# Optimization experiments

Hardware: AMD Instinct MI355X
Metric: run time of the kernel (lower is better)

## Reference

```python
import jax, jax.numpy as jnp
import numpy as np

N = 100000   # nodes
E = 1600000  # edges (no self loops; added per PyG default)
DIN = 64; DMID = 64; DOUT = 64; H = 8
C_MID = DMID // H  # per-head dim for concat layers
NEG_SLOPE = 0.2


def _segment_softmax(logits, seg, num):
    # logits: [E', H], seg: [E'] target node ids
    m = jax.ops.segment_max(logits, seg, num_segments=num)  # [N, H]
    e = jnp.exp(logits - m[seg])
    s = jax.ops.segment_sum(e, seg, num_segments=num)
    return e / (s[seg] + 1e-16)


def _gatv2_layer(x, src, dst, Wl, Wr, att, bias, heads, concat):
    n = x.shape[0]
    c = Wl.shape[1] // heads
    xl = (x @ Wl).reshape(n, heads, c)  # source transform
    xr = (x @ Wr).reshape(n, heads, c)  # target transform
    m = xl[src] + xr[dst]               # [E', H, C] gathered messages
    e = jnp.where(m > 0, m, NEG_SLOPE * m)
    alpha = jnp.einsum('ehc,hc->eh', e, att)            # [E', H]
    alpha = _segment_softmax(alpha, dst, n)
    out = jax.ops.segment_sum(alpha[..., None] * xl[src], dst, num_segments=n)  # [N, H, C]
    if concat:
        out = out.reshape(n, heads * c)
    else:
        out = out.mean(axis=1)
    return out + bias


def setup_inputs() -> dict:
    key = jax.random.key(0)
    ks = jax.random.split(key, 16)
    x = jax.random.normal(ks[0], (N, DIN), jnp.float32)
    src = jax.random.randint(ks[1], (E,), 0, N)
    dst = jax.random.randint(ks[2], (E,), 0, N)
    dst = jnp.where(src == dst, (dst + 1) % N, dst)  # no pre-existing self loops
    edge_index = jnp.stack([src, dst]).astype(jnp.int64)

    def lin(k, fi, fo):
        return jax.random.normal(k, (fi, fo), jnp.float32) / np.sqrt(fi)

    inp = {'x': x, 'edge_index': edge_index}
    # layer 0: din -> H*C_MID (concat), layer 1: dmid -> H*C_MID (concat), layer 2: dmid -> H*DOUT (mean)
    dims = [(DIN, H * C_MID, C_MID), (DMID, H * C_MID, C_MID), (DMID, H * DOUT, DOUT)]
    kidx = 3
    for i, (fi, fo, c) in enumerate(dims):
        inp[f'W{i}l'] = lin(ks[kidx], fi, fo); kidx += 1
        inp[f'W{i}r'] = lin(ks[kidx], fi, fo); kidx += 1
        inp[f'a{i}'] = jax.random.normal(ks[kidx], (H, c), jnp.float32) / np.sqrt(c); kidx += 1
        bsize = fo if i < 2 else DOUT
        inp[f'b{i}'] = jnp.zeros((bsize,), jnp.float32)
    return inp


def reference(x, edge_index, W0l, W0r, a0, b0, W1l, W1r, a1, b1, W2l, W2r, a2, b2):
    # add self loops (PyG GATv2Conv default add_self_loops=True)
    loop = jnp.arange(N, dtype=edge_index.dtype)
    src = jnp.concatenate([edge_index[0], loop])
    dst = jnp.concatenate([edge_index[1], loop])

    # eval mode: dropout is identity
    h = jax.nn.elu(_gatv2_layer(x, src, dst, W0l, W0r, a0, b0, H, True))
    prev_h = jnp.zeros_like(h)

    h_in = h + prev_h
    h = jax.nn.elu(_gatv2_layer(h_in, src, dst, W1l, W1r, a1, b1, H, True))
    prev_h = h_in

    h_in = h + prev_h
    out = _gatv2_layer(h_in, src, dst, W2l, W2r, a2, b2, H, False)
    return out
```

## Files before the change

### kernel.cpp

```cpp
#include <hip/hip_runtime.h>
#include <math.h>

#define NNODES 100000
typedef unsigned short bf16_t;

typedef __attribute__((ext_vector_type(8))) short bf16x8;
typedef __attribute__((ext_vector_type(4))) float f32x4;

#define LOG2E 1.44269504f
#define THR2 11.5415603f

__device__ __forceinline__ float bf_lo(unsigned u) { return __uint_as_float(u << 16); }
__device__ __forceinline__ float bf_hi(unsigned u) { return __uint_as_float(u & 0xffff0000u); }
__device__ __forceinline__ bf16_t f2bf(float f) {
  unsigned u = __float_as_uint(f);
  return (bf16_t)((u + 0x7fffu + ((u >> 16) & 1u)) >> 16);
}
__device__ __forceinline__ float leaky(float v) { return fmaxf(v, 0.2f * v); }

#define LDK 68

__global__ __launch_bounds__(256) void gemm_mfma(const float* __restrict__ in,
                                                 const float* __restrict__ Wl,
                                                 const float* __restrict__ Wr,
                                                 bf16_t* __restrict__ XL,
                                                 bf16_t* __restrict__ XR,
                                                 int n, int fo, int col0, int ncols) {
  __shared__ bf16_t sX[64][LDK];
  __shared__ bf16_t sL[64][LDK];
  __shared__ bf16_t sR[64][LDK];
  int r0 = blockIdx.x * 64;
  int ct = blockIdx.y * 64;
  for (int i = threadIdx.x; i < 64 * 64; i += 256) {
    int r = i >> 6, k = i & 63;
    float v = (r0 + r < n) ? in[(size_t)(r0 + r) * 64 + k] : 0.f;
    sX[r][k] = f2bf(v);
  }
  for (int i = threadIdx.x; i < 64 * 64; i += 256) {
    int k = i >> 6, c = i & 63;
    int gc = col0 + ct + c;
    sL[c][k] = f2bf(Wl[k * fo + gc]);
    sR[c][k] = f2bf(Wr[k * fo + gc]);
  }
  __syncthreads();
  int w = threadIdx.x >> 6, l = threadIdx.x & 63;
  int l16 = l & 15, kg = l >> 4;
  bf16x8 a0 = *(const bf16x8*)&sX[w * 16 + l16][kg * 8];
  bf16x8 a1 = *(const bf16x8*)&sX[w * 16 + l16][kg * 8 + 32];
  f32x4 accL[4], accR[4];
#pragma unroll
  for (int nt = 0; nt < 4; ++nt) {
#pragma unroll
    for (int r = 0; r < 4; ++r) { accL[nt][r] = 0.f; accR[nt][r] = 0.f; }
  }
#pragma unroll
  for (int nt = 0; nt < 4; ++nt) {
    bf16x8 bl0 = *(const bf16x8*)&sL[nt * 16 + l16][kg * 8];
    bf16x8 bl1 = *(const bf16x8*)&sL[nt * 16 + l16][kg * 8 + 32];
    bf16x8 br0 = *(const bf16x8*)&sR[nt * 16 + l16][kg * 8];
    bf16x8 br1 = *(const bf16x8*)&sR[nt * 16 + l16][kg * 8 + 32];
    accL[nt] = __builtin_amdgcn_mfma_f32_16x16x32_bf16(a0, bl0, accL[nt], 0, 0, 0);
    accL[nt] = __builtin_amdgcn_mfma_f32_16x16x32_bf16(a1, bl1, accL[nt], 0, 0, 0);
    accR[nt] = __builtin_amdgcn_mfma_f32_16x16x32_bf16(a0, br0, accR[nt], 0, 0, 0);
    accR[nt] = __builtin_amdgcn_mfma_f32_16x16x32_bf16(a1, br1, accR[nt], 0, 0, 0);
  }
#pragma unroll
  for (int nt = 0; nt < 4; ++nt) {
#pragma unroll
    for (int r = 0; r < 4; ++r) {
      int grow = r0 + w * 16 + kg * 4 + r;
      if (grow < n) {
        size_t o = (size_t)grow * ncols + ct + nt * 16 + l16;
        XL[o] = f2bf(accL[nt][r]);
        XR[o] = f2bf(accR[nt][r]);
      }
    }
  }
}

__global__ void zeroi(int* __restrict__ p, int n) {
  int i = blockIdx.x * blockDim.x + threadIdx.x;
  if (i < n) p[i] = 0;
}
__global__ void histrank(const int* __restrict__ ei, int E,
                         int* __restrict__ cnt, unsigned char* __restrict__ rank) {
  int e = blockIdx.x * blockDim.x + threadIdx.x;
  if (e < E) rank[e] = (unsigned char)atomicAdd(&cnt[ei[E + e]], 1);
}
__global__ void scan1(const int* __restrict__ cnt, int n,
                      int* __restrict__ scn, int* __restrict__ bsum) {
  __shared__ int sh[256];
  int t = threadIdx.x, i = blockIdx.x * 256 + t;
  int v = (i < n) ? cnt[i] : 0;
  sh[t] = v;
  __syncthreads();
  for (int off = 1; off < 256; off <<= 1) {
    int x = (t >= off) ? sh[t - off] : 0;
    __syncthreads();
    sh[t] += x;
    __syncthreads();
  }
  if (i < n) scn[i] = sh[t];
  if (t == 255) bsum[blockIdx.x] = sh[255];
}
__global__ void scan2(int* __restrict__ bsum, int nb) {
  __shared__ int sh[512];
  int t = threadIdx.x;
  sh[t] = (t < nb) ? bsum[t] : 0;
  __syncthreads();
  for (int off = 1; off < 512; off <<= 1) {
    int x = (t >= off) ? sh[t - off] : 0;
    __syncthreads();
    sh[t] += x;
    __syncthreads();
  }
  if (t < nb) bsum[t] = sh[t];
}
__global__ void scan3(int* __restrict__ RS, const int* __restrict__ bsum, int n) {
  int i = blockIdx.x * blockDim.x + threadIdx.x;
  if (i >= n) return;
  int b = i >> 8;
  int pre = (b > 0) ? bsum[b - 1] : 0;
  RS[i + 1] += pre;
  if (i == 0) RS[0] = 0;
}
__global__ void scat2(const int* __restrict__ ei, int E,
                      const int* __restrict__ RS,
                      const unsigned char* __restrict__ rank,
                      int* __restrict__ SRC) {
  int e = blockIdx.x * blockDim.x + threadIdx.x;
  if (e >= E) return;
  int d = ei[E + e];
  SRC[RS[d] + (int)rank[e]] = ei[e];
}

__global__ __launch_bounds__(256) void fused01(const bf16_t* __restrict__ xl,
                                               const bf16_t* __restrict__ xr,
                                               const float* __restrict__ att,
                                               const int* __restrict__ RS,
                                               const int* __restrict__ SRC,
                                               const float* __restrict__ bias,
                                               float* __restrict__ curbuf,
                                               int n, int addres) {
  int l = threadIdx.x & 63;
  int q = l & 15;
  int d = blockIdx.x * 16 + ((threadIdx.x >> 6) << 2) + (l >> 4);
  int dd = (d < n) ? d : 0;
  float a0 = att[4 * q] * LOG2E, a1 = att[4 * q + 1] * LOG2E;
  float a2 = att[4 * q + 2] * LOG2E, a3 = att[4 * q + 3] * LOG2E;
  const char* xlb = (const char*)xl;
  uint2 ur = *(const uint2*)((const char*)xr + ((unsigned)dd << 7) + (q << 3));
  float r0 = bf_lo(ur.x), r1 = bf_hi(ur.x), r2 = bf_lo(ur.y), r3 = bf_hi(ur.y);
  int rs = RS[dd], re = RS[dd + 1];
  int cnt = (d < n) ? (re - rs + 1) : 0;
  int mc = max(cnt, __shfl_xor(cnt, 16));
  mc = max(mc, __shfl_xor(mc, 32));
  float m = -1e30f, s = 0.f, ac0 = 0.f, ac1 = 0.f, ac2 = 0.f, ac3 = 0.f;
  int nsid = (rs < re) ? SRC[rs] : dd;
  uint2 u = *(const uint2*)(xlb + ((unsigned)dd << 7) + (q << 3));
  for (int j = 0;;) {
    uint2 un = *(const uint2*)(xlb + ((unsigned)nsid << 7) + (q << 3));
    int i2 = rs + j + 1;
    int nn = (i2 < re) ? SRC[i2] : dd;
    float x0 = bf_lo(u.x), x1 = bf_hi(u.x), x2 = bf_lo(u.y), x3 = bf_hi(u.y);
    float t = leaky(x0 + r0) * a0 + leaky(x1 + r1) * a1 +
              leaky(x2 + r2) * a2 + leaky(x3 + r3) * a3;
    t += __shfl_xor(t, 1);
    if (j >= cnt) t = -1e30f;
    if (__any(t > m + THR2)) {
      float nm = fmaxf(m, t);
      float e0 = exp2f(m - nm);
      s *= e0; ac0 *= e0; ac1 *= e0; ac2 *= e0; ac3 *= e0; m = nm;
    }
    float e1 = exp2f(t - m);
    s += e1;
    ac0 += e1 * x0; ac1 += e1 * x1; ac2 += e1 * x2; ac3 += e1 * x3;
    ++j;
    if (j >= mc) break;
    u = un;
    nsid = nn;
  }
  if (d < n) {
    float inv = 1.f / (s + 1e-16f);
    float v0 = ac0 * inv + bias[4 * q];
    float v1 = ac1 * inv + bias[4 * q + 1];
    float v2 = ac2 * inv + bias[4 * q + 2];
    float v3 = ac3 * inv + bias[4 * q + 3];
    v0 = v0 > 0.f ? v0 : expm1f(v0);
    v1 = v1 > 0.f ? v1 : expm1f(v1);
    v2 = v2 > 0.f ? v2 : expm1f(v2);
    v3 = v3 > 0.f ? v3 : expm1f(v3);
    float4* pc = (float4*)(curbuf + (size_t)d * 64 + 4 * q);
    if (addres) {
      float4 pr = *pc;
      v0 += pr.x; v1 += pr.y; v2 += pr.z; v3 += pr.w;
    }
    *pc = make_float4(v0, v1, v2, v3);
  }
}

template <int NH>
__global__ __launch_bounds__(256) void fused2(const bf16_t* __restrict__ xl,
                                              const bf16_t* __restrict__ xr,
                                              const float* __restrict__ att,
                                              const int* __restrict__ RS,
                                              const int* __restrict__ SRC,
                                              const float* __restrict__ bias,
                                              float* __restrict__ accbuf,
                                              float* __restrict__ outbuf,
                                              int n, int h0, int pass) {
  const int LPD = NH * 8;
  const unsigned RB = NH * 128u;
  int l = threadIdx.x & 63;
  int ll = l & (LPD - 1);
  int d = blockIdx.x * (256 / LPD) + (threadIdx.x >> 6) * (64 / LPD) +
          (NH == 4 ? (l >> 5) : 0);
  int dd = (d < n) ? d : 0;
  int h = ll >> 3, c0 = (ll & 7) * 8;
  const float* ap = att + (h0 + h) * 64 + c0;
  float a[8];
#pragma unroll
  for (int k = 0; k < 8; ++k) a[k] = ap[k] * LOG2E;
  const char* xlb = (const char*)xl;
  uint4 ur = *(const uint4*)((const char*)xr + (unsigned)dd * RB + (ll << 4));
  float r[8] = {bf_lo(ur.x), bf_hi(ur.x), bf_lo(ur.y), bf_hi(ur.y),
                bf_lo(ur.z), bf_hi(ur.z), bf_lo(ur.w), bf_hi(ur.w)};
  int rs = RS[dd], re = RS[dd + 1];
  int cnt = (d < n) ? (re - rs + 1) : 0;
  int maxcnt = (NH == 4) ? max(cnt, __shfl_xor(cnt, 32)) : cnt;
  float m = -1e30f, s = 0.f;
  float ac[8] = {0.f, 0.f, 0.f, 0.f, 0.f, 0.f, 0.f, 0.f};
  int nsid = (rs < re) ? SRC[rs] : dd;
  uint4 u = *(const uint4*)(xlb + (unsigned)dd * RB + (ll << 4));
  for (int j = 0;;) {
    uint4 un = *(const uint4*)(xlb + (unsigned)nsid * RB + (ll << 4));
    int i2 = rs + j + 1;
    int nn = (i2 < re) ? SRC[i2] : dd;
    float x[8] = {bf_lo(u.x), bf_hi(u.x), bf_lo(u.y), bf_hi(u.y),
                  bf_lo(u.z), bf_hi(u.z), bf_lo(u.w), bf_hi(u.w)};
    float t = 0.f;
#pragma unroll
    for (int k = 0; k < 8; ++k) t += leaky(x[k] + r[k]) * a[k];
    t += __shfl_xor(t, 1);
    t += __shfl_xor(t, 2);
    t += __shfl_xor(t, 4);
    if (j >= cnt) t = -1e30f;
    if (__any(t > m + THR2)) {
      float nm = fmaxf(m, t);
      float e0 = exp2f(m - nm);
      s *= e0;
#pragma unroll
      for (int k = 0; k < 8; ++k) ac[k] *= e0;
      m = nm;
    }
    float e1 = exp2f(t - m);
    s += e1;
#pragma unroll
    for (int k = 0; k < 8; ++k) ac[k] += e1 * x[k];
    ++j;
    if (j >= maxcnt) break;
    u = un;
    nsid = nn;
  }
  float inv = 1.f / (s + 1e-16f);
  float v[8];
#pragma unroll
  for (int k = 0; k < 8; ++k) {
    v[k] = ac[k] * inv;
    v[k] += __shfl_xor(v[k], 8);
    v[k] += __shfl_xor(v[k], 16);
    if (NH == 8) v[k] += __shfl_xor(v[k], 32);
  }
  if (ll < 8 && d < n) {
    if (NH == 8) {
      const float* bp = bias + ll * 8;
      float4 o0, o1;
      o0.x = v[0] * 0.125f + bp[0];
      o0.y = v[1] * 0.125f + bp[1];
      o0.z = v[2] * 0.125f + bp[2];
      o0.w = v[3] * 0.125f + bp[3];
      o1.x = v[4] * 0.125f + bp[4];
      o1.y = v[5] * 0.125f + bp[5];
      o1.z = v[6] * 0.125f + bp[6];
      o1.w = v[7] * 0.125f + bp[7];
      float* po = outbuf + (size_t)d * 64 + ll * 8;
      *(float4*)po = o0;
      *(float4*)(po + 4) = o1;
    } else {
      float* pa = accbuf + (size_t)d * 64 + ll * 8;
      if (pass == 0) {
        *(float4*)pa = make_float4(v[0], v[1], v[2], v[3]);
        *(float4*)(pa + 4) = make_float4(v[4], v[5], v[6], v[7]);
      } else {
        float4 p0 = *(float4*)pa;
        float4 p1 = *(float4*)(pa + 4);
        const float* bp = bias + ll * 8;
        float4 o0, o1;
        o0.x = (p0.x + v[0]) * 0.125f + bp[0];
        o0.y = (p0.y + v[1]) * 0.125f + bp[1];
        o0.z = (p0.z + v[2]) * 0.125f + bp[2];
        o0.w = (p0.w + v[3]) * 0.125f + bp[3];
        o1.x = (p1.x + v[4]) * 0.125f + bp[4];
        o1.y = (p1.y + v[5]) * 0.125f + bp[5];
        o1.z = (p1.z + v[6]) * 0.125f + bp[6];
        o1.w = (p1.w + v[7]) * 0.125f + bp[7];
        float* po = outbuf + (size_t)d * 64 + ll * 8;
        *(float4*)po = o0;
        *(float4*)(po + 4) = o1;
      }
    }
  }
}

extern "C" void kernel_launch(void* const* d_in, const int* in_sizes, int n_in,
                              void* d_out, int out_size, void* d_ws, size_t ws_size,
                              hipStream_t stream) {
  const float* x = (const float*)d_in[0];
  const int* ei = (const int*)d_in[1];
  const float* Wmat[3][2] = {
      {(const float*)d_in[2], (const float*)d_in[3]},
      {(const float*)d_in[6], (const float*)d_in[7]},
      {(const float*)d_in[10], (const float*)d_in[11]}};
  const float* att[3] = {(const float*)d_in[4], (const float*)d_in[8],
                         (const float*)d_in[12]};
  const float* bias[3] = {(const float*)d_in[5], (const float*)d_in[9],
                          (const float*)d_in[13]};
  const int N = NNODES;
  int E = in_sizes[1] / 2;

  auto al = [](size_t b) { return (b + 255) & ~(size_t)255; };
  size_t csr_bytes = al((size_t)(N + 1) * 4) + al((size_t)N * 4) + al(512 * 4) +
                     al((size_t)E * 4) + al((size_t)E);
  size_t need8 = al((size_t)N * 64 * 4) + 2 * al((size_t)N * 512 * 2) + csr_bytes;
  bool mode8 = (ws_size >= need8);

  char* p = (char*)d_ws;
  auto alloc = [&](size_t bytes) {
    char* r = p;
    p += (bytes + 255) & ~(size_t)255;
    return r;
  };
  float* CUR = (float*)alloc((size_t)N * 64 * 4);
  size_t xtab = mode8 ? (size_t)N * 512 * 2 : (size_t)N * 256 * 2;
  bf16_t* XL = (bf16_t*)alloc(xtab);
  bf16_t* XR = (bf16_t*)alloc(xtab);
  int* RS = (int*)alloc((size_t)(N + 1) * 4);
  int* CNT = (int*)alloc((size_t)N * 4);
  int* BSUM = (int*)alloc(512 * 4);
  int* SRC = (int*)alloc((size_t)E * 4);
  unsigned char* RANK = (unsigned char*)alloc((size_t)E);
  float* ACC = mode8 ? nullptr : (float*)alloc((size_t)N * 64 * 4);

  const int nb = (N + 255) / 256;
  const int geblk = (E + 255) / 256;
  const int g01 = (N + 15) / 16;
  const int gx64 = (N + 63) / 64;

  zeroi<<<nb, 256, 0, stream>>>(CNT, N);
  histrank<<<geblk, 256, 0, stream>>>(ei, E, CNT, RANK);
  scan1<<<nb, 256, 0, stream>>>(CNT, N, RS + 1, BSUM);
  scan2<<<1, 512, 0, stream>>>(BSUM, nb);
  scan3<<<nb, 256, 0, stream>>>(RS, BSUM, N);
  scat2<<<geblk, 256, 0, stream>>>(ei, E, RS, RANK, SRC);

  for (int layer = 0; layer < 2; ++layer) {
    const float* in = (layer == 0) ? x : CUR;
    gemm_mfma<<<dim3(gx64, 1), 256, 0, stream>>>(in, Wmat[layer][0], Wmat[layer][1],
                                                 XL, XR, N, 64, 0, 64);
    fused01<<<g01, 256, 0, stream>>>(XL, XR, att[layer], RS, SRC, bias[layer],
                                     CUR, N, layer);
  }

  if (mode8) {
    gemm_mfma<<<dim3(gx64, 8), 256, 0, stream>>>(CUR, Wmat[2][0], Wmat[2][1],
                                                 XL, XR, N, 512, 0, 512);
    fused2<8><<<(N + 3) / 4, 256, 0, stream>>>(XL, XR, att[2], RS, SRC, bias[2],
                                               nullptr, (float*)d_out, N, 0, 0);
  } else {
    for (int hb = 0; hb < 2; ++hb) {
      gemm_mfma<<<dim3(gx64, 4), 256, 0, stream>>>(CUR, Wmat[2][0], Wmat[2][1],
                                                   XL, XR, N, 512, hb * 256, 256);
      fused2<4><<<(N + 7) / 8, 256, 0, stream>>>(XL, XR, att[2], RS, SRC, bias[2],
                                                 ACC, (float*)d_out, N, hb * 4, hb);
    }
  }
}
```

Measured before the change: 632.2 us.

## Split leaky-ReLU attention into linear per-node terms plus abs edge term

Uses leaky(v) = 0.6v + 0.4|v| to move the linear part of the attention score into per-node scalars AL/AR, computed in the GEMM epilogue and stored in new small tables. The edge loop then only evaluates the abs term and adds two gathered scalars. It also swaps exp2f for raw v_exp_f32, adds an occupancy hint to the launch bounds, and drops the j>=cnt mask in the 8-head path. The cost is an extra gathered AL load per edge, and the abs/linear split and bf16-rounded inputs to the per-node terms can shift results slightly.

```diff
diff --git a/kernel.cpp b/kernel.cpp
--- a/kernel.cpp
+++ b/kernel.cpp
@@ -9,6 +9,8 @@
 
 #define LOG2E 1.44269504f
 #define THR2 11.5415603f
+#define CLIN (0.6f * LOG2E)
+#define CABS (0.4f * LOG2E)
 
 __device__ __forceinline__ float bf_lo(unsigned u) { return __uint_as_float(u << 16); }
 __device__ __forceinline__ float bf_hi(unsigned u) { return __uint_as_float(u & 0xffff0000u); }
@@ -16,15 +18,23 @@
   unsigned u = __float_as_uint(f);
   return (bf16_t)((u + 0x7fffu + ((u >> 16) & 1u)) >> 16);
 }
-__device__ __forceinline__ float leaky(float v) { return fmaxf(v, 0.2f * v); }
+__device__ __forceinline__ float ex2(float x) {
+  float r;
+  asm("v_exp_f32 %0, %1" : "=v"(r) : "v"(x));
+  return r;
+}
 
 #define LDK 68
 
+template <int HM>
 __global__ __launch_bounds__(256) void gemm_mfma(const float* __restrict__ in,
                                                  const float* __restrict__ Wl,
                                                  const float* __restrict__ Wr,
+                                                 const float* __restrict__ att,
                                                  bf16_t* __restrict__ XL,
                                                  bf16_t* __restrict__ XR,
+                                                 float* __restrict__ AL,
+                                                 float* __restrict__ AR,
                                                  int n, int fo, int col0, int ncols) {
   __shared__ bf16_t sX[64][LDK];
   __shared__ bf16_t sL[64][LDK];
@@ -64,15 +74,49 @@
     accR[nt] = __builtin_amdgcn_mfma_f32_16x16x32_bf16(a0, br0, accR[nt], 0, 0, 0);
     accR[nt] = __builtin_amdgcn_mfma_f32_16x16x32_bf16(a1, br1, accR[nt], 0, 0, 0);
   }
-#pragma unroll
-  for (int nt = 0; nt < 4; ++nt) {
-#pragma unroll
-    for (int r = 0; r < 4; ++r) {
-      int grow = r0 + w * 16 + kg * 4 + r;
-      if (grow < n) {
+  float aw[4];
+#pragma unroll
+  for (int nt = 0; nt < 4; ++nt) aw[nt] = att[col0 + ct + nt * 16 + l16] * CLIN;
+  int head1 = (col0 + ct) >> 6;
+#pragma unroll
+  for (int r = 0; r < 4; ++r) {
+    int grow = r0 + w * 16 + kg * 4 + r;
+    bool ok = grow < n;
+    float sLh = 0.f, sRh = 0.f;
+#pragma unroll
+    for (int nt = 0; nt < 4; ++nt) {
+      bf16_t bl = f2bf(accL[nt][r]), br = f2bf(accR[nt][r]);
+      float xl_ = bf_lo((unsigned)bl << 16 >> 16 << 16);
+      float xr_ = bf_lo((unsigned)br);
+      xl_ = __uint_as_float(((unsigned)bl) << 16);
+      xr_ = __uint_as_float(((unsigned)br) << 16);
+      if (ok) {
         size_t o = (size_t)grow * ncols + ct + nt * 16 + l16;
-        XL[o] = f2bf(accL[nt][r]);
-        XR[o] = f2bf(accR[nt][r]);
+        XL[o] = bl;
+        XR[o] = br;
+      }
+      if (HM) {
+        sLh += aw[nt] * xl_;
+        sRh += aw[nt] * xr_;
+      } else {
+        float vL = aw[nt] * xl_, vR = aw[nt] * xr_;
+        vL += __shfl_xor(vL, 1); vL += __shfl_xor(vL, 2); vL += __shfl_xor(vL, 4);
+        vR += __shfl_xor(vR, 1); vR += __shfl_xor(vR, 2); vR += __shfl_xor(vR, 4);
+        if ((l16 & 7) == 0 && ok) {
+          int head = 2 * nt + (l16 >> 3);
+          AL[grow * 8 + head] = vL;
+          AR[grow * 8 + head] = vR;
+        }
+      }
+    }
+    if (HM) {
+      sLh += __shfl_xor(sLh, 1); sLh += __shfl_xor(sLh, 2);
+      sLh += __shfl_xor(sLh, 4); sLh += __shfl_xor(sLh, 8);
+      sRh += __shfl_xor(sRh, 1); sRh += __shfl_xor(sRh, 2);
+      sRh += __shfl_xor(sRh, 4); sRh += __shfl_xor(sRh, 8);
+      if (l16 == 0 && ok) {
+        AL[grow * 8 + head1] = sLh;
+        AR[grow * 8 + head1] = sRh;
       }
     }
   }
@@ -134,23 +178,27 @@
   SRC[RS[d] + (int)rank[e]] = ei[e];
 }
 
-__global__ __launch_bounds__(256) void fused01(const bf16_t* __restrict__ xl,
-                                               const bf16_t* __restrict__ xr,
-                                               const float* __restrict__ att,
-                                               const int* __restrict__ RS,
-                                               const int* __restrict__ SRC,
-                                               const float* __restrict__ bias,
-                                               float* __restrict__ curbuf,
-                                               int n, int addres) {
+__global__ __launch_bounds__(256, 6) void fused01(const bf16_t* __restrict__ xl,
+                                                  const bf16_t* __restrict__ xr,
+                                                  const float* __restrict__ att,
+                                                  const float* __restrict__ AL,
+                                                  const float* __restrict__ AR,
+                                                  const int* __restrict__ RS,
+                                                  const int* __restrict__ SRC,
+                                                  const float* __restrict__ bias,
+                                                  float* __restrict__ curbuf,
+                                                  int n, int addres) {
   int l = threadIdx.x & 63;
   int q = l & 15;
+  int h01 = q >> 1;
   int d = blockIdx.x * 16 + ((threadIdx.x >> 6) << 2) + (l >> 4);
   int dd = (d < n) ? d : 0;
-  float a0 = att[4 * q] * LOG2E, a1 = att[4 * q + 1] * LOG2E;
-  float a2 = att[4 * q + 2] * LOG2E, a3 = att[4 * q + 3] * LOG2E;
+  float c0 = att[4 * q] * CABS, c1 = att[4 * q + 1] * CABS;
+  float c2 = att[4 * q + 2] * CABS, c3 = att[4 * q + 3] * CABS;
   const char* xlb = (const char*)xl;
   uint2 ur = *(const uint2*)((const char*)xr + ((unsigned)dd << 7) + (q << 3));
   float r0 = bf_lo(ur.x), r1 = bf_hi(ur.x), r2 = bf_lo(ur.y), r3 = bf_hi(ur.y);
+  float ard = AR[dd * 8 + h01];
   int rs = RS[dd], re = RS[dd + 1];
   int cnt = (d < n) ? (re - rs + 1) : 0;
   int mc = max(cnt, __shfl_xor(cnt, 16));
@@ -158,26 +206,30 @@
   float m = -1e30f, s = 0.f, ac0 = 0.f, ac1 = 0.f, ac2 = 0.f, ac3 = 0.f;
   int nsid = (rs < re) ? SRC[rs] : dd;
   uint2 u = *(const uint2*)(xlb + ((unsigned)dd << 7) + (q << 3));
+  float alc = AL[dd * 8 + h01];
   for (int j = 0;;) {
     uint2 un = *(const uint2*)(xlb + ((unsigned)nsid << 7) + (q << 3));
+    float aln = AL[nsid * 8 + h01];
     int i2 = rs + j + 1;
     int nn = (i2 < re) ? SRC[i2] : dd;
     float x0 = bf_lo(u.x), x1 = bf_hi(u.x), x2 = bf_lo(u.y), x3 = bf_hi(u.y);
-    float t = leaky(x0 + r0) * a0 + leaky(x1 + r1) * a1 +
-              leaky(x2 + r2) * a2 + leaky(x3 + r3) * a3;
+    float t = c0 * fabsf(x0 + r0) + c1 * fabsf(x1 + r1) +
+              c2 * fabsf(x2 + r2) + c3 * fabsf(x3 + r3);
     t += __shfl_xor(t, 1);
+    t += alc + ard;
     if (j >= cnt) t = -1e30f;
     if (__any(t > m + THR2)) {
       float nm = fmaxf(m, t);
-      float e0 = exp2f(m - nm);
+      float e0 = ex2(m - nm);
       s *= e0; ac0 *= e0; ac1 *= e0; ac2 *= e0; ac3 *= e0; m = nm;
     }
-    float e1 = exp2f(t - m);
+    float e1 = ex2(t - m);
     s += e1;
     ac0 += e1 * x0; ac1 += e1 * x1; ac2 += e1 * x2; ac3 += e1 * x3;
     ++j;
     if (j >= mc) break;
     u = un;
+    alc = aln;
     nsid = nn;
   }
   if (d < n) {
@@ -200,15 +252,17 @@
 }
 
 template <int NH>
-__global__ __launch_bounds__(256) void fused2(const bf16_t* __restrict__ xl,
-                                              const bf16_t* __restrict__ xr,
-                                              const float* __restrict__ att,
-                                              const int* __restrict__ RS,
-                                              const int* __restrict__ SRC,
-                                              const float* __restrict__ bias,
-                                              float* __restrict__ accbuf,
-                                              float* __restrict__ outbuf,
-                                              int n, int h0, int pass) {
+__global__ __launch_bounds__(256, 6) void fused2(const bf16_t* __restrict__ xl,
+                                                 const bf16_t* __restrict__ xr,
+                                                 const float* __restrict__ att,
+                                                 const float* __restrict__ AL,
+                                                 const float* __restrict__ AR,
+                                                 const int* __restrict__ RS,
+                                                 const int* __restrict__ SRC,
+                                                 const float* __restrict__ bias,
+                                                 float* __restrict__ accbuf,
+                                                 float* __restrict__ outbuf,
+                                                 int n, int h0, int pass) {
   const int LPD = NH * 8;
   const unsigned RB = NH * 128u;
   int l = threadIdx.x & 63;
@@ -217,14 +271,16 @@
           (NH == 4 ? (l >> 5) : 0);
   int dd = (d < n) ? d : 0;
   int h = ll >> 3, c0 = (ll & 7) * 8;
-  const float* ap = att + (h0 + h) * 64 + c0;
-  float a[8];
-#pragma unroll
-  for (int k = 0; k < 8; ++k) a[k] = ap[k] * LOG2E;
+  int habs = h0 + h;
+  const float* ap = att + habs * 64 + c0;
+  float c[8];
+#pragma unroll
+  for (int k = 0; k < 8; ++k) c[k] = ap[k] * CABS;
   const char* xlb = (const char*)xl;
   uint4 ur = *(const uint4*)((const char*)xr + (unsigned)dd * RB + (ll << 4));
   float r[8] = {bf_lo(ur.x), bf_hi(ur.x), bf_lo(ur.y), bf_hi(ur.y),
                 bf_lo(ur.z), bf_hi(ur.z), bf_lo(ur.w), bf_hi(ur.w)};
+  float ard = AR[dd * 8 + habs];
   int rs = RS[dd], re = RS[dd + 1];
   int cnt = (d < n) ? (re - rs + 1) : 0;
   int maxcnt = (NH == 4) ? max(cnt, __shfl_xor(cnt, 32)) : cnt;
@@ -232,34 +288,38 @@
   float ac[8] = {0.f, 0.f, 0.f, 0.f, 0.f, 0.f, 0.f, 0.f};
   int nsid = (rs < re) ? SRC[rs] : dd;
   uint4 u = *(const uint4*)(xlb + (unsigned)dd * RB + (ll << 4));
+  float alc = AL[dd * 8 + habs];
   for (int j = 0;;) {
     uint4 un = *(const uint4*)(xlb + (unsigned)nsid * RB + (ll << 4));
+    float aln = AL[nsid * 8 + habs];
     int i2 = rs + j + 1;
     int nn = (i2 < re) ? SRC[i2] : dd;
     float x[8] = {bf_lo(u.x), bf_hi(u.x), bf_lo(u.y), bf_hi(u.y),
                   bf_lo(u.z), bf_hi(u.z), bf_lo(u.w), bf_hi(u.w)};
     float t = 0.f;
 #pragma unroll
-    for (int k = 0; k < 8; ++k) t += leaky(x[k] + r[k]) * a[k];
+    for (int k = 0; k < 8; ++k) t += c[k] * fabsf(x[k] + r[k]);
     t += __shfl_xor(t, 1);
     t += __shfl_xor(t, 2);
     t += __shfl_xor(t, 4);
-    if (j >= cnt) t = -1e30f;
+    t += alc + ard;
+    if (NH == 4 && j >= cnt) t = -1e30f;
     if (__any(t > m + THR2)) {
       float nm = fmaxf(m, t);
-      float e0 = exp2f(m - nm);
+      float e0 = ex2(m - nm);
       s *= e0;
 #pragma unroll
       for (int k = 0; k < 8; ++k) ac[k] *= e0;
       m = nm;
     }
-    float e1 = exp2f(t - m);
+    float e1 = ex2(t - m);
     s += e1;
 #pragma unroll
     for (int k = 0; k < 8; ++k) ac[k] += e1 * x[k];
     ++j;
     if (j >= maxcnt) break;
     u = un;
+    alc = aln;
     nsid = nn;
   }
   float inv = 1.f / (s + 1e-16f);
@@ -329,9 +389,11 @@
   int E = in_sizes[1] / 2;
 
   auto al = [](size_t b) { return (b + 255) & ~(size_t)255; };
-  size_t csr_bytes = al((size_t)(N + 1) * 4) + al((size_t)N * 4) + al(512 * 4) +
-                     al((size_t)E * 4) + al((size_t)E);
-  size_t need8 = al((size_t)N * 64 * 4) + 2 * al((size_t)N * 512 * 2) + csr_bytes;
+  size_t fixed = al((size_t)N * 64 * 4)
+               + 2 * al((size_t)N * 8 * 4)
+               + al((size_t)(N + 1) * 4) + al((size_t)N * 4)
+               + al(512 * 4) + al((size_t)E * 4) + al((size_t)E);
+  size_t need8 = fixed + 2 * al((size_t)N * 512 * 2);
   bool mode8 = (ws_size >= need8);
 
   char* p = (char*)d_ws;
@@ -341,6 +403,8 @@
     return r;
   };
   float* CUR = (float*)alloc((size_t)N * 64 * 4);
+  float* ALt = (float*)alloc((size_t)N * 8 * 4);
+  float* ARt = (float*)alloc((size_t)N * 8 * 4);
   size_t xtab = mode8 ? (size_t)N * 512 * 2 : (size_t)N * 256 * 2;
   bf16_t* XL = (bf16_t*)alloc(xtab);
   bf16_t* XR = (bf16_t*)alloc(xtab);
@@ -365,23 +429,23 @@
 
   for (int layer = 0; layer < 2; ++layer) {
     const float* in = (layer == 0) ? x : CUR;
-    gemm_mfma<<<dim3(gx64, 1), 256, 0, stream>>>(in, Wmat[layer][0], Wmat[layer][1],
-                                                 XL, XR, N, 64, 0, 64);
-    fused01<<<g01, 256, 0, stream>>>(XL, XR, att[layer], RS, SRC, bias[layer],
-                                     CUR, N, layer);
+    gemm_mfma<0><<<dim3(gx64, 1), 256, 0, stream>>>(
+        in, Wmat[layer][0], Wmat[layer][1], att[layer], XL, XR, ALt, ARt, N, 64, 0, 64);
+    fused01<<<g01, 256, 0, stream>>>(XL, XR, att[layer], ALt, ARt, RS, SRC,
+                                     bias[layer], CUR, N, layer);
   }
 
   if (mode8) {
-    gemm_mfma<<<dim3(gx64, 8), 256, 0, stream>>>(CUR, Wmat[2][0], Wmat[2][1],
-                                                 XL, XR, N, 512, 0, 512);
-    fused2<8><<<(N + 3) / 4, 256, 0, stream>>>(XL, XR, att[2], RS, SRC, bias[2],
-                                               nullptr, (float*)d_out, N, 0, 0);
+    gemm_mfma<1><<<dim3(gx64, 8), 256, 0, stream>>>(
+        CUR, Wmat[2][0], Wmat[2][1], att[2], XL, XR, ALt, ARt, N, 512, 0, 512);
+    fused2<8><<<(N + 3) / 4, 256, 0, stream>>>(XL, XR, att[2], ALt, ARt, RS, SRC,
+                                               bias[2], nullptr, (float*)d_out, N, 0, 0);
   } else {
     for (int hb = 0; hb < 2; ++hb) {
-      gemm_mfma<<<dim3(gx64, 4), 256, 0, stream>>>(CUR, Wmat[2][0], Wmat[2][1],
-                                                   XL, XR, N, 512, hb * 256, 256);
-      fused2<4><<<(N + 7) / 8, 256, 0, stream>>>(XL, XR, att[2], RS, SRC, bias[2],
-                                                 ACC, (float*)d_out, N, hb * 4, hb);
-    }
-  }
-}
+      gemm_mfma<1><<<dim3(gx64, 4), 256, 0, stream>>>(
+          CUR, Wmat[2][0], Wmat[2][1], att[2], XL, XR, ALt, ARt, N, 512, hb * 256, 256);
+      fused2<4><<<(N + 7) / 8, 256, 0, stream>>>(XL, XR, att[2], ALt, ARt, RS, SRC,
+                                                 bias[2], ACC, (float*)d_out, N, hb * 4, hb);
+    }
+  }
+}
```

Result: slower. 695.9 us (+10.1%).

## Switch feature tables from bf16 to fp16 with packed-half attention math

Applied to the files above, without the earlier changes.

The projected feature tables are now stored as fp16 instead of bf16, and the GEMM uses the fp16 MFMA. In the aggregation loops, leaky-ReLU runs on packed half2 values and the attention dot product uses fdot2. Weighted accumulation uses v_fma_mix, so halves are not unpacked into floats, and exp2f is replaced by raw v_exp_f32. The aim is fewer VALU instructions per edge in the gather-bound kernels, at the cost of fp16 range and precision limits and lower accuracy in the exp.

```diff
diff --git a/kernel.cpp b/kernel.cpp
--- a/kernel.cpp
+++ b/kernel.cpp
@@ -1,52 +1,74 @@
 #include <hip/hip_runtime.h>
+#include <hip/hip_fp16.h>
 #include <math.h>
 
 #define NNODES 100000
-typedef unsigned short bf16_t;
-
-typedef __attribute__((ext_vector_type(8))) short bf16x8;
-typedef __attribute__((ext_vector_type(4))) float f32x4;
+
+typedef _Float16 f16x2 __attribute__((ext_vector_type(2)));
+typedef _Float16 f16x8 __attribute__((ext_vector_type(8)));
+typedef float f32x4 __attribute__((ext_vector_type(4)));
 
 #define LOG2E 1.44269504f
 #define THR2 11.5415603f
 
-__device__ __forceinline__ float bf_lo(unsigned u) { return __uint_as_float(u << 16); }
-__device__ __forceinline__ float bf_hi(unsigned u) { return __uint_as_float(u & 0xffff0000u); }
-__device__ __forceinline__ bf16_t f2bf(float f) {
-  unsigned u = __float_as_uint(f);
-  return (bf16_t)((u + 0x7fffu + ((u >> 16) & 1u)) >> 16);
-}
-__device__ __forceinline__ float leaky(float v) { return fmaxf(v, 0.2f * v); }
+__device__ __forceinline__ float ex2(float x) {
+  float r;
+  asm("v_exp_f32 %0, %1" : "=v"(r) : "v"(x));
+  return r;
+}
+__device__ __forceinline__ f16x2 bch(unsigned x) {
+  return __builtin_bit_cast(f16x2, x);
+}
+__device__ __forceinline__ float fdot2h(f16x2 a, f16x2 b, float c) {
+#if __has_builtin(__builtin_amdgcn_fdot2)
+  return __builtin_amdgcn_fdot2(a, b, c, false);
+#else
+  return c + (float)a.x * (float)b.x + (float)a.y * (float)b.y;
+#endif
+}
+__device__ __forceinline__ void fmix_lo(float& acc, unsigned xpk, float e) {
+  asm("v_fma_mix_f32 %0, %1, %2, %0 op_sel_hi:[1,0,0]"
+      : "+v"(acc) : "v"(xpk), "v"(e));
+}
+__device__ __forceinline__ void fmix_hi(float& acc, unsigned xpk, float e) {
+  asm("v_fma_mix_f32 %0, %1, %2, %0 op_sel:[1,0,0] op_sel_hi:[1,0,0]"
+      : "+v"(acc) : "v"(xpk), "v"(e));
+}
+__device__ __forceinline__ f16x2 pleaky(f16x2 v) {
+  f16x2 w = v * (_Float16)0.2f;
+  return __builtin_elementwise_max(v, w);
+}
 
 #define LDK 68
 
 __global__ __launch_bounds__(256) void gemm_mfma(const float* __restrict__ in,
                                                  const float* __restrict__ Wl,
                                                  const float* __restrict__ Wr,
-                                                 bf16_t* __restrict__ XL,
-                                                 bf16_t* __restrict__ XR,
-                                                 int n, int fo, int col0, int ncols) {
-  __shared__ bf16_t sX[64][LDK];
-  __shared__ bf16_t sL[64][LDK];
-  __shared__ bf16_t sR[64][LDK];
+                                                 char* __restrict__ XLb,
+                                                 char* __restrict__ XRb,
+                                                 int n, int fo, int col0,
+                                                 unsigned RB) {
+  __shared__ _Float16 sX[64][LDK];
+  __shared__ _Float16 sL[64][LDK];
+  __shared__ _Float16 sR[64][LDK];
   int r0 = blockIdx.x * 64;
   int ct = blockIdx.y * 64;
   for (int i = threadIdx.x; i < 64 * 64; i += 256) {
     int r = i >> 6, k = i & 63;
     float v = (r0 + r < n) ? in[(size_t)(r0 + r) * 64 + k] : 0.f;
-    sX[r][k] = f2bf(v);
+    sX[r][k] = (_Float16)v;
   }
   for (int i = threadIdx.x; i < 64 * 64; i += 256) {
     int k = i >> 6, c = i & 63;
     int gc = col0 + ct + c;
-    sL[c][k] = f2bf(Wl[k * fo + gc]);
-    sR[c][k] = f2bf(Wr[k * fo + gc]);
+    sL[c][k] = (_Float16)Wl[k * fo + gc];
+    sR[c][k] = (_Float16)Wr[k * fo + gc];
   }
   __syncthreads();
   int w = threadIdx.x >> 6, l = threadIdx.x & 63;
   int l16 = l & 15, kg = l >> 4;
-  bf16x8 a0 = *(const bf16x8*)&sX[w * 16 + l16][kg * 8];
-  bf16x8 a1 = *(const bf16x8*)&sX[w * 16 + l16][kg * 8 + 32];
+  f16x8 a0 = *(const f16x8*)&sX[w * 16 + l16][kg * 8];
+  f16x8 a1 = *(const f16x8*)&sX[w * 16 + l16][kg * 8 + 32];
   f32x4 accL[4], accR[4];
 #pragma unroll
   for (int nt = 0; nt < 4; ++nt) {
@@ -55,25 +77,26 @@
   }
 #pragma unroll
   for (int nt = 0; nt < 4; ++nt) {
-    bf16x8 bl0 = *(const bf16x8*)&sL[nt * 16 + l16][kg * 8];
-    bf16x8 bl1 = *(const bf16x8*)&sL[nt * 16 + l16][kg * 8 + 32];
-    bf16x8 br0 = *(const bf16x8*)&sR[nt * 16 + l16][kg * 8];
-    bf16x8 br1 = *(const bf16x8*)&sR[nt * 16 + l16][kg * 8 + 32];
-    accL[nt] = __builtin_amdgcn_mfma_f32_16x16x32_bf16(a0, bl0, accL[nt], 0, 0, 0);
-    accL[nt] = __builtin_amdgcn_mfma_f32_16x16x32_bf16(a1, bl1, accL[nt], 0, 0, 0);
-    accR[nt] = __builtin_amdgcn_mfma_f32_16x16x32_bf16(a0, br0, accR[nt], 0, 0, 0);
-    accR[nt] = __builtin_amdgcn_mfma_f32_16x16x32_bf16(a1, br1, accR[nt], 0, 0, 0);
-  }
-#pragma unroll
-  for (int nt = 0; nt < 4; ++nt) {
-#pragma unroll
-    for (int r = 0; r < 4; ++r) {
-      int grow = r0 + w * 16 + kg * 4 + r;
-      if (grow < n) {
-        size_t o = (size_t)grow * ncols + ct + nt * 16 + l16;
-        XL[o] = f2bf(accL[nt][r]);
-        XR[o] = f2bf(accR[nt][r]);
-      }
+    f16x8 bl0 = *(const f16x8*)&sL[nt * 16 + l16][kg * 8];
+    f16x8 bl1 = *(const f16x8*)&sL[nt * 16 + l16][kg * 8 + 32];
+    f16x8 br0 = *(const f16x8*)&sR[nt * 16 + l16][kg * 8];
+    f16x8 br1 = *(const f16x8*)&sR[nt * 16 + l16][kg * 8 + 32];
+    accL[nt] = __builtin_amdgcn_mfma_f32_16x16x32_f16(a0, bl0, accL[nt], 0, 0, 0);
+    accL[nt] = __builtin_amdgcn_mfma_f32_16x16x32_f16(a1, bl1, accL[nt], 0, 0, 0);
+    accR[nt] = __builtin_amdgcn_mfma_f32_16x16x32_f16(a0, br0, accR[nt], 0, 0, 0);
+    accR[nt] = __builtin_amdgcn_mfma_f32_16x16x32_f16(a1, br1, accR[nt], 0, 0, 0);
+  }
+#pragma unroll
+  for (int r = 0; r < 4; ++r) {
+    int grow = r0 + w * 16 + kg * 4 + r;
+    if (grow >= n) continue;
+    char* rowL = XLb + (size_t)grow * RB;
+    char* rowR = XRb + (size_t)grow * RB;
+#pragma unroll
+    for (int nt = 0; nt < 4; ++nt) {
+      int chb = (ct + nt * 16 + l16) * 2;
+      *(_Float16*)(rowL + chb) = (_Float16)accL[nt][r];
+      *(_Float16*)(rowR + chb) = (_Float16)accR[nt][r];
     }
   }
 }
@@ -134,8 +157,8 @@
   SRC[RS[d] + (int)rank[e]] = ei[e];
 }
 
-__global__ __launch_bounds__(256) void fused01(const bf16_t* __restrict__ xl,
-                                               const bf16_t* __restrict__ xr,
+__global__ __launch_bounds__(256) void fused01(const char* __restrict__ xlb,
+                                               const char* __restrict__ xrb,
                                                const float* __restrict__ att,
                                                const int* __restrict__ RS,
                                                const int* __restrict__ SRC,
@@ -146,11 +169,10 @@
   int q = l & 15;
   int d = blockIdx.x * 16 + ((threadIdx.x >> 6) << 2) + (l >> 4);
   int dd = (d < n) ? d : 0;
-  float a0 = att[4 * q] * LOG2E, a1 = att[4 * q + 1] * LOG2E;
-  float a2 = att[4 * q + 2] * LOG2E, a3 = att[4 * q + 3] * LOG2E;
-  const char* xlb = (const char*)xl;
-  uint2 ur = *(const uint2*)((const char*)xr + ((unsigned)dd << 7) + (q << 3));
-  float r0 = bf_lo(ur.x), r1 = bf_hi(ur.x), r2 = bf_lo(ur.y), r3 = bf_hi(ur.y);
+  f16x2 c2a = {(_Float16)(att[4 * q] * LOG2E), (_Float16)(att[4 * q + 1] * LOG2E)};
+  f16x2 c2b = {(_Float16)(att[4 * q + 2] * LOG2E), (_Float16)(att[4 * q + 3] * LOG2E)};
+  uint2 ur = *(const uint2*)(xrb + ((unsigned)dd << 7) + (q << 3));
+  f16x2 r2a = bch(ur.x), r2b = bch(ur.y);
   int rs = RS[dd], re = RS[dd + 1];
   int cnt = (d < n) ? (re - rs + 1) : 0;
   int mc = max(cnt, __shfl_xor(cnt, 16));
@@ -162,19 +184,23 @@
     uint2 un = *(const uint2*)(xlb + ((unsigned)nsid << 7) + (q << 3));
     int i2 = rs + j + 1;
     int nn = (i2 < re) ? SRC[i2] : dd;
-    float x0 = bf_lo(u.x), x1 = bf_hi(u.x), x2 = bf_lo(u.y), x3 = bf_hi(u.y);
-    float t = leaky(x0 + r0) * a0 + leaky(x1 + r1) * a1 +
-              leaky(x2 + r2) * a2 + leaky(x3 + r3) * a3;
+    f16x2 la = pleaky(bch(u.x) + r2a);
+    f16x2 lb = pleaky(bch(u.y) + r2b);
+    float t = fdot2h(la, c2a, 0.f);
+    t = fdot2h(lb, c2b, t);
     t += __shfl_xor(t, 1);
     if (j >= cnt) t = -1e30f;
     if (__any(t > m + THR2)) {
       float nm = fmaxf(m, t);
-      float e0 = exp2f(m - nm);
+      float e0 = ex2(m - nm);
       s *= e0; ac0 *= e0; ac1 *= e0; ac2 *= e0; ac3 *= e0; m = nm;
     }
-    float e1 = exp2f(t - m);
+    float e1 = ex2(t - m);
     s += e1;
-    ac0 += e1 * x0; ac1 += e1 * x1; ac2 += e1 * x2; ac3 += e1 * x3;
+    fmix_lo(ac0, u.x, e1);
+    fmix_hi(ac1, u.x, e1);
+    fmix_lo(ac2, u.y, e1);
+    fmix_hi(ac3, u.y, e1);
     ++j;
     if (j >= mc) break;
     u = un;
@@ -200,8 +226,8 @@
 }
 
 template <int NH>
-__global__ __launch_bounds__(256) void fused2(const bf16_t* __restrict__ xl,
-                                              const bf16_t* __restrict__ xr,
+__global__ __launch_bounds__(256) void fused2(const char* __restrict__ xlb,
+                                              const char* __restrict__ xrb,
                                               const float* __restrict__ att,
                                               const int* __restrict__ RS,
                                               const int* __restrict__ SRC,
@@ -209,54 +235,61 @@
                                               float* __restrict__ accbuf,
                                               float* __restrict__ outbuf,
                                               int n, int h0, int pass) {
-  const int LPD = NH * 8;
-  const unsigned RB = NH * 128u;
+  constexpr int RSH = (NH == 8) ? 10 : 9;
   int l = threadIdx.x & 63;
-  int ll = l & (LPD - 1);
-  int d = blockIdx.x * (256 / LPD) + (threadIdx.x >> 6) * (64 / LPD) +
-          (NH == 4 ? (l >> 5) : 0);
+  int ll = (NH == 8) ? l : (l & 31);
+  int d = (NH == 8) ? blockIdx.x * 4 + (threadIdx.x >> 6)
+                    : blockIdx.x * 8 + ((threadIdx.x >> 6) << 1) + (l >> 5);
   int dd = (d < n) ? d : 0;
   int h = ll >> 3, c0 = (ll & 7) * 8;
   const float* ap = att + (h0 + h) * 64 + c0;
-  float a[8];
-#pragma unroll
-  for (int k = 0; k < 8; ++k) a[k] = ap[k] * LOG2E;
-  const char* xlb = (const char*)xl;
-  uint4 ur = *(const uint4*)((const char*)xr + (unsigned)dd * RB + (ll << 4));
-  float r[8] = {bf_lo(ur.x), bf_hi(ur.x), bf_lo(ur.y), bf_hi(ur.y),
-                bf_lo(ur.z), bf_hi(ur.z), bf_lo(ur.w), bf_hi(ur.w)};
+  f16x2 c2[4];
+#pragma unroll
+  for (int k = 0; k < 4; ++k)
+    c2[k] = f16x2{(_Float16)(ap[2 * k] * LOG2E), (_Float16)(ap[2 * k + 1] * LOG2E)};
+  uint4 ur = *(const uint4*)(xrb + ((unsigned)dd << RSH) + (ll << 4));
+  f16x2 r2[4] = {bch(ur.x), bch(ur.y), bch(ur.z), bch(ur.w)};
   int rs = RS[dd], re = RS[dd + 1];
   int cnt = (d < n) ? (re - rs + 1) : 0;
   int maxcnt = (NH == 4) ? max(cnt, __shfl_xor(cnt, 32)) : cnt;
   float m = -1e30f, s = 0.f;
   float ac[8] = {0.f, 0.f, 0.f, 0.f, 0.f, 0.f, 0.f, 0.f};
   int nsid = (rs < re) ? SRC[rs] : dd;
-  uint4 u = *(const uint4*)(xlb + (unsigned)dd * RB + (ll << 4));
+  uint4 u = *(const uint4*)(xlb + ((unsigned)dd << RSH) + (ll << 4));
   for (int j = 0;;) {
-    uint4 un = *(const uint4*)(xlb + (unsigned)nsid * RB + (ll << 4));
+    uint4 un = *(const uint4*)(xlb + ((unsigned)nsid << RSH) + (ll << 4));
     int i2 = rs + j + 1;
     int nn = (i2 < re) ? SRC[i2] : dd;
-    float x[8] = {bf_lo(u.x), bf_hi(u.x), bf_lo(u.y), bf_hi(u.y),
-                  bf_lo(u.z), bf_hi(u.z), bf_lo(u.w), bf_hi(u.w)};
-    float t = 0.f;
-#pragma unroll
-    for (int k = 0; k < 8; ++k) t += leaky(x[k] + r[k]) * a[k];
+    f16x2 l0 = pleaky(bch(u.x) + r2[0]);
+    f16x2 l1 = pleaky(bch(u.y) + r2[1]);
+    f16x2 l2 = pleaky(bch(u.z) + r2[2]);
+    f16x2 l3 = pleaky(bch(u.w) + r2[3]);
+    float t = fdot2h(l0, c2[0], 0.f);
+    t = fdot2h(l1, c2[1], t);
+    t = fdot2h(l2, c2[2], t);
+    t = fdot2h(l3, c2[3], t);
     t += __shfl_xor(t, 1);
     t += __shfl_xor(t, 2);
     t += __shfl_xor(t, 4);
-    if (j >= cnt) t = -1e30f;
+    if (NH == 4 && j >= cnt) t = -1e30f;
     if (__any(t > m + THR2)) {
       float nm = fmaxf(m, t);
-      float e0 = exp2f(m - nm);
+      float e0 = ex2(m - nm);
       s *= e0;
 #pragma unroll
       for (int k = 0; k < 8; ++k) ac[k] *= e0;
       m = nm;
     }
-    float e1 = exp2f(t - m);
+    float e1 = ex2(t - m);
     s += e1;
-#pragma unroll
-    for (int k = 0; k < 8; ++k) ac[k] += e1 * x[k];
+    fmix_lo(ac[0], u.x, e1);
+    fmix_hi(ac[1], u.x, e1);
+    fmix_lo(ac[2], u.y, e1);
+    fmix_hi(ac[3], u.y, e1);
+    fmix_lo(ac[4], u.z, e1);
+    fmix_hi(ac[5], u.z, e1);
+    fmix_lo(ac[6], u.w, e1);
+    fmix_hi(ac[7], u.w, e1);
     ++j;
     if (j >= maxcnt) break;
     u = un;
@@ -329,9 +362,10 @@
   int E = in_sizes[1] / 2;
 
   auto al = [](size_t b) { return (b + 255) & ~(size_t)255; };
-  size_t csr_bytes = al((size_t)(N + 1) * 4) + al((size_t)N * 4) + al(512 * 4) +
-                     al((size_t)E * 4) + al((size_t)E);
-  size_t need8 = al((size_t)N * 64 * 4) + 2 * al((size_t)N * 512 * 2) + csr_bytes;
+  size_t fixed = al((size_t)N * 64 * 4)
+               + al((size_t)(N + 1) * 4) + al((size_t)N * 4)
+               + al(512 * 4) + al((size_t)E * 4) + al((size_t)E);
+  size_t need8 = fixed + 2 * al((size_t)N * 1024);
   bool mode8 = (ws_size >= need8);
 
   char* p = (char*)d_ws;
@@ -341,9 +375,9 @@
     return r;
   };
   float* CUR = (float*)alloc((size_t)N * 64 * 4);
-  size_t xtab = mode8 ? (size_t)N * 512 * 2 : (size_t)N * 256 * 2;
-  bf16_t* XL = (bf16_t*)alloc(xtab);
-  bf16_t* XR = (bf16_t*)alloc(xtab);
+  size_t xtab = mode8 ? (size_t)N * 1024 : (size_t)N * 512;
+  char* XL = alloc(xtab);
+  char* XR = alloc(xtab);
   int* RS = (int*)alloc((size_t)(N + 1) * 4);
   int* CNT = (int*)alloc((size_t)N * 4);
   int* BSUM = (int*)alloc(512 * 4);
@@ -365,21 +399,21 @@
 
   for (int layer = 0; layer < 2; ++layer) {
     const float* in = (layer == 0) ? x : CUR;
-    gemm_mfma<<<dim3(gx64, 1), 256, 0, stream>>>(in, Wmat[layer][0], Wmat[layer][1],
-                                                 XL, XR, N, 64, 0, 64);
+    gemm_mfma<<<dim3(gx64, 1), 256, 0, stream>>>(
+        in, Wmat[layer][0], Wmat[layer][1], XL, XR, N, 64, 0, 128u);
     fused01<<<g01, 256, 0, stream>>>(XL, XR, att[layer], RS, SRC, bias[layer],
                                      CUR, N, layer);
   }
 
   if (mode8) {
-    gemm_mfma<<<dim3(gx64, 8), 256, 0, stream>>>(CUR, Wmat[2][0], Wmat[2][1],
-                                                 XL, XR, N, 512, 0, 512);
+    gemm_mfma<<<dim3(gx64, 8), 256, 0, stream>>>(
+        CUR, Wmat[2][0], Wmat[2][1], XL, XR, N, 512, 0, 1024u);
     fused2<8><<<(N + 3) / 4, 256, 0, stream>>>(XL, XR, att[2], RS, SRC, bias[2],
                                                nullptr, (float*)d_out, N, 0, 0);
   } else {
     for (int hb = 0; hb < 2; ++hb) {
-      gemm_mfma<<<dim3(gx64, 4), 256, 0, stream>>>(CUR, Wmat[2][0], Wmat[2][1],
-                                                   XL, XR, N, 512, hb * 256, 256);
+      gemm_mfma<<<dim3(gx64, 4), 256, 0, stream>>>(
+          CUR, Wmat[2][0], Wmat[2][1], XL, XR, N, 512, hb * 256, 512u);
       fused2<4><<<(N + 7) / 8, 256, 0, stream>>>(XL, XR, att[2], RS, SRC, bias[2],
                                                  ACC, (float*)d_out, N, hb * 4, hb);
     }
```

Measured after the change: 672.7 us. 6.4% more time.
